# Kernel tuning notes

Hardware: AMD Instinct MI355X
Metric: run time of the kernel (lower is better)

## Reference

```python
import jax, jax.numpy as jnp
import numpy as np

PS = 32
D = 256


def setup_inputs() -> dict:
    key = jax.random.key(0)
    ks = jax.random.split(key, 9)
    B, L = 32, 32768
    s_in = 1.0 / np.sqrt(PS)
    s_d = 1.0 / np.sqrt(D)
    return {
        "x": jax.random.normal(ks[0], (B, L), dtype=jnp.float32),
        "W_proj": jax.random.normal(ks[1], (PS, D), dtype=jnp.float32) * s_in,
        "b_proj": jnp.zeros((D,), jnp.float32),
        "W_qkv": jax.random.normal(ks[2], (D, 3 * D), dtype=jnp.float32) * s_d,
        "b_qkv": jnp.zeros((3 * D,), jnp.float32),
        "W_out": jax.random.normal(ks[3], (D, D), dtype=jnp.float32) * s_d,
        "b_out": jnp.zeros((D,), jnp.float32),
        "W_head": jax.random.normal(ks[4], (D, PS), dtype=jnp.float32) * s_d,
        "b_head": jnp.zeros((PS,), jnp.float32),
    }


def reference(x, W_proj, b_proj, W_qkv, b_qkv, W_out, b_out, W_head, b_head):
    B, L = x.shape
    T = L // PS
    # InstanceNorm over full series (torch .std is unbiased -> ddof=1)
    mean = jnp.mean(x, axis=-1, keepdims=True)
    std = jnp.std(x, axis=-1, keepdims=True, ddof=1) + 1e-5
    x_norm = (x - mean) / std
    patches = x_norm.reshape(B, T, PS)
    # Patch embedding
    h = patches @ W_proj + b_proj  # [B, T, D]
    # Single-head causal self-attention (explicit scores, as in source)
    qkv = h @ W_qkv + b_qkv
    q, k, v = jnp.split(qkv, 3, axis=-1)
    scale = 1.0 / jnp.sqrt(jnp.asarray(D, dtype=h.dtype))
    attn = jnp.einsum("btd,bsd->bts", q, k) * scale  # [B, T, T]
    causal = jnp.tril(jnp.ones((T, T), dtype=bool))
    attn = jnp.where(causal, attn, -jnp.inf)
    attn = jax.nn.softmax(attn, axis=-1)
    out = jnp.einsum("bts,bsd->btd", attn, v)
    out = out @ W_out + b_out
    # Prediction head + next-patch MSE loss
    pred = out @ W_head + b_head  # [B, T, PS]
    loss = jnp.mean((pred[:, :-1] - patches[:, 1:]) ** 2)
    return loss
```

## Files before the change

### kernel.cpp

```cpp
#include <hip/hip_runtime.h>
#include <math.h>

#define B_SZ 32
#define L_SZ 32768
#define T_SZ 1024
#define PS_SZ 32
#define D_SZ 256
#define SM_M 10.0f

typedef float f32x4 __attribute__((ext_vector_type(4)));
typedef short s16x8 __attribute__((ext_vector_type(8)));
typedef unsigned short u16x8 __attribute__((ext_vector_type(8)));

__device__ __forceinline__ unsigned short f2bf(float f) {
  union { float f; unsigned int u; } v; v.f = f;
  unsigned int r = v.u + 0x7FFFu + ((v.u >> 16) & 1u);
  return (unsigned short)(r >> 16);
}

__device__ __forceinline__ void g2l16(const unsigned short* g, unsigned short* l) {
  __builtin_amdgcn_global_load_lds(
      (const __attribute__((address_space(1))) unsigned int*)g,
      (__attribute__((address_space(3))) unsigned int*)l, 16, 0, 0);
}

__global__ __launch_bounds__(256) void prep_kernel(const float* __restrict__ x,
                                                   float* __restrict__ sgpart,
                                                   const float* __restrict__ Wp,
                                                   const float* __restrict__ bp,
                                                   const float* __restrict__ Wq,
                                                   const float* __restrict__ bq,
                                                   const float* __restrict__ Wo,
                                                   const float* __restrict__ bo,
                                                   const float* __restrict__ Wh,
                                                   const float* __restrict__ bh,
                                                   float* __restrict__ Wcb,
                                                   unsigned short* __restrict__ WqT,
                                                   unsigned short* __restrict__ WfT,
                                                   float* __restrict__ bfp,
                                                   unsigned int* __restrict__ total,
                                                   float* __restrict__ lsum) {
  __shared__ float red[8];
  const int g = blockIdx.x, tid = threadIdx.x;
  const int w = tid >> 6, lane = tid & 63;
  if (g < 256) {
    const int b = g >> 3;
    const float* p = x + (size_t)b * L_SZ + (size_t)(g & 7) * 4096;
    float s = 0.f, ss = 0.f;
#pragma unroll
    for (int i = 0; i < 4; ++i) {
      float4 f = ((const float4*)p)[tid + i * 256];
      s += f.x + f.y + f.z + f.w;
      ss += f.x * f.x + f.y * f.y + f.z * f.z + f.w * f.w;
    }
#pragma unroll
    for (int off = 32; off >= 1; off >>= 1) {
      s += __shfl_down(s, off);
      ss += __shfl_down(ss, off);
    }
    if (lane == 0) { red[w] = s; red[4 + w] = ss; }
    __syncthreads();
    if (tid == 0) {
      sgpart[g * 2]     = red[0] + red[1] + red[2] + red[3];
      sgpart[g * 2 + 1] = red[4] + red[5] + red[6] + red[7];
    }
  } else if (g < 388) {
    int idx = (g - 256) * 256 + tid;
    if (idx < 33 * 768) {
      int p = idx / 768, j = idx % 768;
      const float* arow = (p < 32) ? (Wp + p * 256) : bp;
      float acc = (p < 32) ? 0.f : bq[j];
      for (int d = 0; d < 256; ++d) acc += arow[d] * Wq[d * 768 + j];
      if (p < 32) WqT[j * 32 + p] = f2bf(acc);
      else Wcb[j] = acc;
    } else {
      int k = idx - 33 * 768;
      if (k < 8192) {
        int p = k >> 8, d = k & 255;
        float acc = 0.f;
        for (int e = 0; e < 256; ++e) acc += Wo[d * 256 + e] * Wh[e * 32 + p];
        WfT[p * 256 + d] = f2bf(acc);
      } else if (k < 8224) {
        int p = k - 8192;
        float acc = bh[p];
        for (int e = 0; e < 256; ++e) acc += bo[e] * Wh[e * 32 + p];
        bfp[p] = acc;
      }
    }
  } else {
    if (tid == 0) { total[0] = 0u; lsum[0] = 0.f; }
  }
}

__global__ __launch_bounds__(256) void qkv_kernel(const float* __restrict__ x,
                                                  const float* __restrict__ sgpart,
                                                  const unsigned short* __restrict__ WqT,
                                                  const float* __restrict__ Wcb,
                                                  unsigned short* __restrict__ Qb,
                                                  unsigned short* __restrict__ Kb,
                                                  unsigned short* __restrict__ Vtt) {
  __shared__ unsigned short T4[4][8448];
  const int tid = threadIdx.x;
  const int w = tid >> 6, lane = tid & 63;
  const int lo = lane & 15, quad = lane >> 4;
  unsigned short* Tw = T4[w];
  const int mbase = blockIdx.x * 128 + w * 32;
  const int b = mbase >> 10;
  float S = 0.f, SS = 0.f;
#pragma unroll
  for (int i = 0; i < 8; ++i) {
    S += sgpart[(b * 8 + i) * 2];
    SS += sgpart[(b * 8 + i) * 2 + 1];
  }
  const float mean = S * (1.f / (float)L_SZ);
  const float var = (SS - S * mean) * (1.f / (float)(L_SZ - 1));
  const float inv = 1.f / (sqrtf(var) + 1e-5f);
  s16x8 af0, af1;
  {
    float4 a = *(const float4*)&x[(size_t)(mbase + lo) * 32 + quad * 8];
    float4 c = *(const float4*)&x[(size_t)(mbase + lo) * 32 + quad * 8 + 4];
    af0[0] = (short)f2bf((a.x - mean) * inv); af0[1] = (short)f2bf((a.y - mean) * inv);
    af0[2] = (short)f2bf((a.z - mean) * inv); af0[3] = (short)f2bf((a.w - mean) * inv);
    af0[4] = (short)f2bf((c.x - mean) * inv); af0[5] = (short)f2bf((c.y - mean) * inv);
    af0[6] = (short)f2bf((c.z - mean) * inv); af0[7] = (short)f2bf((c.w - mean) * inv);
    float4 d = *(const float4*)&x[(size_t)(mbase + 16 + lo) * 32 + quad * 8];
    float4 e = *(const float4*)&x[(size_t)(mbase + 16 + lo) * 32 + quad * 8 + 4];
    af1[0] = (short)f2bf((d.x - mean) * inv); af1[1] = (short)f2bf((d.y - mean) * inv);
    af1[2] = (short)f2bf((d.z - mean) * inv); af1[3] = (short)f2bf((d.w - mean) * inv);
    af1[4] = (short)f2bf((e.x - mean) * inv); af1[5] = (short)f2bf((e.y - mean) * inv);
    af1[6] = (short)f2bf((e.z - mean) * inv); af1[7] = (short)f2bf((e.w - mean) * inv);
  }
#pragma unroll 4
  for (int nt = 0; nt < 16; ++nt) {
    s16x8 bf = *(const s16x8*)&WqT[(size_t)(nt * 16 + lo) * 32 + quad * 8];
    f32x4 c0 = {0.f, 0.f, 0.f, 0.f}, c1 = {0.f, 0.f, 0.f, 0.f};
    c0 = __builtin_amdgcn_mfma_f32_16x16x32_bf16(af0, bf, c0, 0, 0, 0);
    c1 = __builtin_amdgcn_mfma_f32_16x16x32_bf16(af1, bf, c1, 0, 0, 0);
    const int col = nt * 16 + lo;
    const float bi = Wcb[col];
#pragma unroll
    for (int i = 0; i < 4; ++i) {
      Tw[(quad * 4 + i) * 264 + col]      = f2bf((c0[i] + bi) * 0.0625f);
      Tw[(16 + quad * 4 + i) * 264 + col] = f2bf((c1[i] + bi) * 0.0625f);
    }
  }
#pragma unroll
  for (int it = 0; it < 16; ++it) {
    const int gsub = it * 64 + lane;
    const int row = gsub >> 5, c16 = gsub & 31;
    *(u16x8*)&Qb[(size_t)(mbase + row) * 256 + c16 * 8] =
        *(const u16x8*)&Tw[row * 264 + c16 * 8];
  }
#pragma unroll 4
  for (int nt = 0; nt < 16; ++nt) {
    s16x8 bf = *(const s16x8*)&WqT[(size_t)(256 + nt * 16 + lo) * 32 + quad * 8];
    f32x4 c0 = {0.f, 0.f, 0.f, 0.f}, c1 = {0.f, 0.f, 0.f, 0.f};
    c0 = __builtin_amdgcn_mfma_f32_16x16x32_bf16(af0, bf, c0, 0, 0, 0);
    c1 = __builtin_amdgcn_mfma_f32_16x16x32_bf16(af1, bf, c1, 0, 0, 0);
    const int col = nt * 16 + lo;
    const float bi = Wcb[256 + col];
#pragma unroll
    for (int i = 0; i < 4; ++i) {
      Tw[(quad * 4 + i) * 264 + col]      = f2bf(c0[i] + bi);
      Tw[(16 + quad * 4 + i) * 264 + col] = f2bf(c1[i] + bi);
    }
  }
#pragma unroll
  for (int it = 0; it < 16; ++it) {
    const int gsub = it * 64 + lane;
    const int row = gsub >> 5, c16 = gsub & 31;
    *(u16x8*)&Kb[(size_t)(mbase + row) * 256 + c16 * 8] =
        *(const u16x8*)&Tw[row * 264 + c16 * 8];
  }
#pragma unroll 4
  for (int nt2 = 0; nt2 < 16; ++nt2) {
    s16x8 aw = *(const s16x8*)&WqT[(size_t)(512 + nt2 * 16 + lo) * 32 + quad * 8];
    f32x4 c0 = {0.f, 0.f, 0.f, 0.f}, c1 = {0.f, 0.f, 0.f, 0.f};
    c0 = __builtin_amdgcn_mfma_f32_16x16x32_bf16(aw, af0, c0, 0, 0, 0);
    c1 = __builtin_amdgcn_mfma_f32_16x16x32_bf16(aw, af1, c1, 0, 0, 0);
#pragma unroll
    for (int i = 0; i < 4; ++i) {
      const int d = nt2 * 16 + quad * 4 + i;
      const float bv = Wcb[512 + d];
      Tw[d * 32 + lo]      = f2bf(c0[i] + bv);
      Tw[d * 32 + 16 + lo] = f2bf(c1[i] + bv);
    }
  }
  {
    const int ktq = (mbase >> 5) & 31;
    const size_t vb = ((size_t)b * 32 + ktq) * 8192;
#pragma unroll
    for (int it = 0; it < 16; ++it) {
      const int gsub = it * 64 + lane;
      *(u16x8*)&Vtt[vb + gsub * 8] = *(const u16x8*)&Tw[gsub * 8];
    }
  }
}

__global__ __launch_bounds__(256) void attn_kernel(const unsigned short* __restrict__ Qb,
                                                   const unsigned short* __restrict__ Kb,
                                                   const unsigned short* __restrict__ Vtt,
                                                   const unsigned short* __restrict__ WfT,
                                                   const float* __restrict__ bfp,
                                                   const float* __restrict__ x,
                                                   const float* __restrict__ sgpart,
                                                   float* __restrict__ lsum,
                                                   unsigned int* __restrict__ total,
                                                   float* __restrict__ out) {
  __shared__ unsigned short SMEM[35328];
  const int g = blockIdx.x;
  const int j = g >> 3;
  const int b = (g & 7) * 4 + (j & 3);
  const int qt = 15 - (j >> 2);
  const int tid = threadIdx.x;
  const int w = tid >> 6, lane = tid & 63;
  const int lo = lane & 15, quad = lane >> 4;

  const int qr0 = qt * 64 + w * 16;
  const size_t kbase = (size_t)b << 10;

  s16x8 qf[8];
  const size_t qrow = (kbase + qr0 + lo) * 256;
#pragma unroll
  for (int kc = 0; kc < 8; ++kc) qf[kc] = *(const s16x8*)&Qb[qrow + kc * 32 + quad * 8];

  f32x4 O[16];
#pragma unroll
  for (int nt = 0; nt < 16; ++nt) O[nt] = (f32x4){0.f, 0.f, 0.f, 0.f};
  f32x4 Ol = {0.f, 0.f, 0.f, 0.f};
  s16x8 ones;
#pragma unroll
  for (int jj = 0; jj < 8; ++jj) ones[jj] = (short)0x3F80;

  const int c16p = tid & 31;
  const int keyr = tid >> 5;
  const int c16s = (c16p & 24) | ((c16p & 7) ^ keyr);
  const unsigned short* kgp = Kb + (kbase << 8) + keyr * 256 + c16s * 8;
  const int dql = tid >> 2;
  const int cpq = (tid & 3) ^ ((tid >> 3) & 3);
  const unsigned short* vgp = Vtt + (size_t)b * 262144 + dql * 32 + cpq * 8;
  const int ldst = (w * 64) * 8;

  unsigned short* myp = &SMEM[32768 + w * 640];
  const int lo7 = lo & 7;
  const int nk = 2 * (qt + 1);

#pragma unroll
  for (int it = 0; it < 4; ++it) g2l16(kgp + it * 2048, &SMEM[it * 2048 + ldst]);
#pragma unroll
  for (int it = 0; it < 4; ++it) g2l16(vgp + it * 2048, &SMEM[8192 + it * 2048 + ldst]);
  kgp += 8192; vgp += 8192;

  for (int kt = 0; kt < nk; ++kt) {
    const int k0 = kt * 32;
    __syncthreads();
    const int cur = (kt & 1) << 14;
    if (kt + 1 < nk) {
      const int nxt = ((kt + 1) & 1) << 14;
#pragma unroll
      for (int it = 0; it < 4; ++it) g2l16(kgp + it * 2048, &SMEM[nxt + it * 2048 + ldst]);
#pragma unroll
      for (int it = 0; it < 4; ++it)
        g2l16(vgp + it * 2048, &SMEM[nxt + 8192 + it * 2048 + ldst]);
      kgp += 8192; vgp += 8192;
    }

    if (k0 <= qr0 + 15) {
      f32x4 s0 = {0.f, 0.f, 0.f, 0.f}, s1 = {0.f, 0.f, 0.f, 0.f};
#pragma unroll
      for (int kc = 0; kc < 8; ++kc) {
        const int c16 = kc * 4 + quad;
        const int cs = (c16 & 24) | ((c16 & 7) ^ lo7);
        s16x8 kf0 = *(const s16x8*)&SMEM[cur + (lo * 32 + cs) * 8];
        s16x8 kf1 = *(const s16x8*)&SMEM[cur + ((16 + lo) * 32 + cs) * 8];
        s0 = __builtin_amdgcn_mfma_f32_16x16x32_bf16(qf[kc], kf0, s0, 0, 0, 0);
        s1 = __builtin_amdgcn_mfma_f32_16x16x32_bf16(qf[kc], kf1, s1, 0, 0, 0);
      }
      if (k0 + 31 > qr0) {
#pragma unroll
        for (int ii = 0; ii < 4; ++ii) {
          const int row = qr0 + quad * 4 + ii;
          if (k0 + lo > row) s0[ii] = -1e30f;
          if (k0 + 16 + lo > row) s1[ii] = -1e30f;
        }
      }
#pragma unroll
      for (int ii = 0; ii < 4; ++ii) {
        myp[(quad * 4 + ii) * 40 + lo]      = f2bf(__expf(s0[ii] - SM_M));
        myp[(quad * 4 + ii) * 40 + 16 + lo] = f2bf(__expf(s1[ii] - SM_M));
      }
      s16x8 pf = *(const s16x8*)&myp[lo * 40 + quad * 8];
      Ol = __builtin_amdgcn_mfma_f32_16x16x32_bf16(pf, ones, Ol, 0, 0, 0);
#pragma unroll
      for (int nt = 0; nt < 16; ++nt) {
        const int d = nt * 16 + lo;
        const int cp = quad ^ ((d >> 1) & 3);
        s16x8 vf = *(const s16x8*)&SMEM[cur + 8192 + ((d << 2) + cp) * 8];
        O[nt] = __builtin_amdgcn_mfma_f32_16x16x32_bf16(pf, vf, O[nt], 0, 0, 0);
      }
    }
  }
  __syncthreads();

  float inv4[4];
#pragma unroll
  for (int ii = 0; ii < 4; ++ii) inv4[ii] = 1.f / Ol[ii];
  unsigned short* OLw = &SMEM[w * 4224];
#pragma unroll
  for (int nt = 0; nt < 16; ++nt)
#pragma unroll
    for (int ii = 0; ii < 4; ++ii)
      OLw[(quad * 4 + ii) * 264 + nt * 16 + lo] = f2bf(O[nt][ii] * inv4[ii]);

  s16x8 af[8];
#pragma unroll
  for (int kc = 0; kc < 8; ++kc)
    af[kc] = *(const s16x8*)&OLw[lo * 264 + kc * 32 + quad * 8];

  float S = 0.f, SS = 0.f;
#pragma unroll
  for (int i = 0; i < 8; ++i) {
    S += sgpart[(b * 8 + i) * 2];
    SS += sgpart[(b * 8 + i) * 2 + 1];
  }
  const float mean = S * (1.f / (float)L_SZ);
  const float var = (SS - S * mean) * (1.f / (float)(L_SZ - 1));
  const float invb = 1.f / (sqrtf(var) + 1e-5f);

  float lacc = 0.f;
#pragma unroll
  for (int nt = 0; nt < 2; ++nt) {
    f32x4 acc = {0.f, 0.f, 0.f, 0.f};
#pragma unroll
    for (int kc = 0; kc < 8; ++kc) {
      s16x8 bfr = *(const s16x8*)&WfT[(size_t)(nt * 16 + lo) * 256 + kc * 32 + quad * 8];
      acc = __builtin_amdgcn_mfma_f32_16x16x32_bf16(af[kc], bfr, acc, 0, 0, 0);
    }
    const float ba = bfp[nt * 16 + lo];
    const int p = nt * 16 + lo;
#pragma unroll
    for (int ii = 0; ii < 4; ++ii) {
      const int t = qr0 + quad * 4 + ii;
      if (t < 1023) {
        const float pr = acc[ii] + ba;
        const float tg = (x[(size_t)b * L_SZ + (t + 1) * 32 + p] - mean) * invb;
        const float d = pr - tg;
        lacc += d * d;
      }
    }
  }
#pragma unroll
  for (int off = 32; off >= 1; off >>= 1) lacc += __shfl_down(lacc, off);
  float* redf = (float*)&SMEM[35000];
  unsigned int* flag = (unsigned int*)&SMEM[35100];
  if (lane == 0) redf[w] = lacc;
  __syncthreads();

  if (tid == 0) {
    atomicAdd(lsum, redf[0] + redf[1] + redf[2] + redf[3]);
    __threadfence();
    unsigned int prev = atomicAdd(total, 1u);
    flag[0] = (prev == 511u) ? 1u : 0u;
  }
  __syncthreads();
  if (flag[0] && tid == 0) {
    float tot = atomicAdd(lsum, 0.0f);
    out[0] = tot * (1.f / (float)(B_SZ * (T_SZ - 1) * PS_SZ));
  }
}

extern "C" void kernel_launch(void* const* d_in, const int* in_sizes, int n_in,
                              void* d_out, int out_size, void* d_ws, size_t ws_size,
                              hipStream_t stream) {
  const float* x      = (const float*)d_in[0];
  const float* W_proj = (const float*)d_in[1];
  const float* b_proj = (const float*)d_in[2];
  const float* W_qkv  = (const float*)d_in[3];
  const float* b_qkv  = (const float*)d_in[4];
  const float* W_out  = (const float*)d_in[5];
  const float* b_out  = (const float*)d_in[6];
  const float* W_head = (const float*)d_in[7];
  const float* b_head = (const float*)d_in[8];
  float* out = (float*)d_out;
  char* ws = (char*)d_ws;

  unsigned short* Qb     = (unsigned short*)ws;
  unsigned short* Kb     = (unsigned short*)(ws + (16ull << 20));
  unsigned short* Vtt    = (unsigned short*)(ws + (32ull << 20));
  char* tail = ws + (48ull << 20);
  float*          Wcb    = (float*)tail;
  unsigned short* WqT    = (unsigned short*)(tail + 4096);
  unsigned short* WfT    = (unsigned short*)(tail + 65536);
  float*          bfp    = (float*)(tail + 98304);
  float*          sgpart = (float*)(tail + 102400);
  unsigned int*   total  = (unsigned int*)(tail + 106496);
  float*          lsum   = (float*)(tail + 106496 + 64);

  prep_kernel<<<389, 256, 0, stream>>>(x, sgpart, W_proj, b_proj, W_qkv, b_qkv,
                                       W_out, b_out, W_head, b_head,
                                       Wcb, WqT, WfT, bfp, total, lsum);
  qkv_kernel<<<256, 256, 0, stream>>>(x, sgpart, WqT, Wcb, Qb, Kb, Vtt);
  attn_kernel<<<512, 256, 0, stream>>>(Qb, Kb, Vtt, WfT, bfp, x, sgpart, lsum, total, out);
}
```

Before: 161.3 us.

## Switch attention to 32x32x16 MFMA with two-wave blocks and reordered tiles

Rewrites the attention kernel so each wave handles 32 query rows using 32x32x16 bf16 MFMA instead of 16x16x32, with 128-thread blocks covering the same 64-row tile. The K, V and P tiles get new LDS swizzles, and the final head projection also uses the larger MFMA. The aim is fewer LDS fragment loads per FLOP and a better MFMA issue rate. The query-tile order across the grid is also changed, and the smaller blocks halve the waves resident per CU, which risks weaker latency hiding.

New measurement: 197.1 us. +22.2%, slower.

```diff
diff --git a/kernel.cpp b/kernel.cpp
--- a/kernel.cpp
+++ b/kernel.cpp
@@ -9,6 +9,7 @@
 #define SM_M 10.0f
 
 typedef float f32x4 __attribute__((ext_vector_type(4)));
+typedef float f32x16 __attribute__((ext_vector_type(16)));
 typedef short s16x8 __attribute__((ext_vector_type(8)));
 typedef unsigned short u16x8 __attribute__((ext_vector_type(8)));
 
@@ -197,59 +198,69 @@
   }
 }
 
-__global__ __launch_bounds__(256) void attn_kernel(const unsigned short* __restrict__ Qb,
-                                                   const unsigned short* __restrict__ Kb,
-                                                   const unsigned short* __restrict__ Vtt,
-                                                   const unsigned short* __restrict__ WfT,
-                                                   const float* __restrict__ bfp,
-                                                   const float* __restrict__ x,
-                                                   const float* __restrict__ sgpart,
-                                                   float* __restrict__ lsum,
-                                                   unsigned int* __restrict__ total,
-                                                   float* __restrict__ out) {
-  __shared__ unsigned short SMEM[35328];
+__global__ __launch_bounds__(128, 1) void attn_kernel(const unsigned short* __restrict__ Qb,
+                                                      const unsigned short* __restrict__ Kb,
+                                                      const unsigned short* __restrict__ Vtt,
+                                                      const unsigned short* __restrict__ WfT,
+                                                      const float* __restrict__ bfp,
+                                                      const float* __restrict__ x,
+                                                      const float* __restrict__ sgpart,
+                                                      float* __restrict__ lsum,
+                                                      unsigned int* __restrict__ total,
+                                                      float* __restrict__ out) {
+  __shared__ unsigned short SMEM[36352];
+  __shared__ float redf[2];
+  __shared__ unsigned int flag;
   const int g = blockIdx.x;
   const int j = g >> 3;
   const int b = (g & 7) * 4 + (j & 3);
-  const int qt = 15 - (j >> 2);
+  const int qt = (j < 32) ? (15 - (j >> 2)) : ((j - 32) >> 2);
   const int tid = threadIdx.x;
   const int w = tid >> 6, lane = tid & 63;
-  const int lo = lane & 15, quad = lane >> 4;
-
-  const int qr0 = qt * 64 + w * 16;
-  const size_t kbase = (size_t)b << 10;
-
-  s16x8 qf[8];
-  const size_t qrow = (kbase + qr0 + lo) * 256;
-#pragma unroll
-  for (int kc = 0; kc < 8; ++kc) qf[kc] = *(const s16x8*)&Qb[qrow + kc * 32 + quad * 8];
-
-  f32x4 O[16];
-#pragma unroll
-  for (int nt = 0; nt < 16; ++nt) O[nt] = (f32x4){0.f, 0.f, 0.f, 0.f};
-  f32x4 Ol = {0.f, 0.f, 0.f, 0.f};
+  const int cl = lane & 31, hi = lane >> 5;
+  const int qr0 = qt * 64 + w * 32;
+
+  s16x8 qf[16];
+  {
+    const size_t qrow = ((size_t)(b * 1024 + qr0 + cl)) * 256;
+#pragma unroll
+    for (int cb = 0; cb < 16; ++cb)
+      qf[cb] = *(const s16x8*)&Qb[qrow + cb * 16 + hi * 8];
+  }
+
+  f32x16 O[8], Ol;
+#pragma unroll
+  for (int dt = 0; dt < 8; ++dt)
+#pragma unroll
+    for (int i = 0; i < 16; ++i) O[dt][i] = 0.f;
+#pragma unroll
+  for (int i = 0; i < 16; ++i) Ol[i] = 0.f;
   s16x8 ones;
 #pragma unroll
   for (int jj = 0; jj < 8; ++jj) ones[jj] = (short)0x3F80;
 
-  const int c16p = tid & 31;
-  const int keyr = tid >> 5;
-  const int c16s = (c16p & 24) | ((c16p & 7) ^ keyr);
-  const unsigned short* kgp = Kb + (kbase << 8) + keyr * 256 + c16s * 8;
-  const int dql = tid >> 2;
-  const int cpq = (tid & 3) ^ ((tid >> 3) & 3);
-  const unsigned short* vgp = Vtt + (size_t)b * 262144 + dql * 32 + cpq * 8;
-  const int ldst = (w * 64) * 8;
-
-  unsigned short* myp = &SMEM[32768 + w * 640];
-  const int lo7 = lo & 7;
+  int kof[8];
+#pragma unroll
+  for (int it = 0; it < 8; ++it) {
+    const int key = it * 4 + (tid >> 5);
+    kof[it] = key * 256 + ((tid & 31) ^ key) * 8;
+  }
+  const int vof = (tid >> 2) * 32 + (((tid & 3) ^ ((tid >> 4) & 3))) * 8;
+  const unsigned short* KbB = Kb + (size_t)b * 262144;
+  const unsigned short* VtB = Vtt + (size_t)b * 262144;
+  const int wb = w * 512;
   const int nk = 2 * (qt + 1);
 
 #pragma unroll
-  for (int it = 0; it < 4; ++it) g2l16(kgp + it * 2048, &SMEM[it * 2048 + ldst]);
-#pragma unroll
-  for (int it = 0; it < 4; ++it) g2l16(vgp + it * 2048, &SMEM[8192 + it * 2048 + ldst]);
-  kgp += 8192; vgp += 8192;
+  for (int it = 0; it < 8; ++it) g2l16(KbB + kof[it], &SMEM[it * 1024 + wb]);
+#pragma unroll
+  for (int it = 0; it < 8; ++it) g2l16(VtB + vof + it * 1024, &SMEM[8192 + it * 1024 + wb]);
+
+  const int maskl = (cl >> 2) & 3;
+  const int cv0 = (hi ^ maskl) * 8;
+  const int cv1 = ((2 | hi) ^ maskl) * 8;
+  unsigned short* Pw = &SMEM[32768 + w * 1792];
+  const int prow = cl * 56;
 
   for (int kt = 0; kt < nk; ++kt) {
     const int k0 = kt * 32;
@@ -257,113 +268,106 @@
     const int cur = (kt & 1) << 14;
     if (kt + 1 < nk) {
       const int nxt = ((kt + 1) & 1) << 14;
-#pragma unroll
-      for (int it = 0; it < 4; ++it) g2l16(kgp + it * 2048, &SMEM[nxt + it * 2048 + ldst]);
-#pragma unroll
-      for (int it = 0; it < 4; ++it)
-        g2l16(vgp + it * 2048, &SMEM[nxt + 8192 + it * 2048 + ldst]);
-      kgp += 8192; vgp += 8192;
-    }
-
-    if (k0 <= qr0 + 15) {
-      f32x4 s0 = {0.f, 0.f, 0.f, 0.f}, s1 = {0.f, 0.f, 0.f, 0.f};
-#pragma unroll
-      for (int kc = 0; kc < 8; ++kc) {
-        const int c16 = kc * 4 + quad;
-        const int cs = (c16 & 24) | ((c16 & 7) ^ lo7);
-        s16x8 kf0 = *(const s16x8*)&SMEM[cur + (lo * 32 + cs) * 8];
-        s16x8 kf1 = *(const s16x8*)&SMEM[cur + ((16 + lo) * 32 + cs) * 8];
-        s0 = __builtin_amdgcn_mfma_f32_16x16x32_bf16(qf[kc], kf0, s0, 0, 0, 0);
-        s1 = __builtin_amdgcn_mfma_f32_16x16x32_bf16(qf[kc], kf1, s1, 0, 0, 0);
+      const int ko = (kt + 1) * 8192;
+#pragma unroll
+      for (int it = 0; it < 8; ++it) g2l16(KbB + ko + kof[it], &SMEM[nxt + it * 1024 + wb]);
+#pragma unroll
+      for (int it = 0; it < 8; ++it)
+        g2l16(VtB + ko + vof + it * 1024, &SMEM[nxt + 8192 + it * 1024 + wb]);
+    }
+
+    if (k0 <= qr0 + 31) {
+      f32x16 S;
+#pragma unroll
+      for (int i = 0; i < 16; ++i) S[i] = 0.f;
+      const int kbl = cur + cl * 256;
+#pragma unroll
+      for (int cb = 0; cb < 16; ++cb) {
+        s16x8 kf = *(const s16x8*)&SMEM[kbl + ((((cb << 1) | hi) ^ cl) << 3)];
+        S = __builtin_amdgcn_mfma_f32_32x32x16_bf16(qf[cb], kf, S, 0, 0, 0);
       }
-      if (k0 + 31 > qr0) {
-#pragma unroll
-        for (int ii = 0; ii < 4; ++ii) {
-          const int row = qr0 + quad * 4 + ii;
-          if (k0 + lo > row) s0[ii] = -1e30f;
-          if (k0 + 16 + lo > row) s1[ii] = -1e30f;
-        }
+      const bool diag = (k0 + 31 > qr0);
+#pragma unroll
+      for (int r = 0; r < 16; ++r) {
+        const int row = (r & 3) + 8 * (r >> 2) + 4 * hi;
+        float e = __expf(S[r] - SM_M);
+        if (diag && (k0 + cl > qr0 + row)) e = 0.f;
+        Pw[row * 56 + cl] = f2bf(e);
       }
-#pragma unroll
-      for (int ii = 0; ii < 4; ++ii) {
-        myp[(quad * 4 + ii) * 40 + lo]      = f2bf(__expf(s0[ii] - SM_M));
-        myp[(quad * 4 + ii) * 40 + 16 + lo] = f2bf(__expf(s1[ii] - SM_M));
+      s16x8 pf0 = *(const s16x8*)&Pw[prow + hi * 8];
+      s16x8 pf1 = *(const s16x8*)&Pw[prow + 16 + hi * 8];
+      Ol = __builtin_amdgcn_mfma_f32_32x32x16_bf16(pf0, ones, Ol, 0, 0, 0);
+      Ol = __builtin_amdgcn_mfma_f32_32x32x16_bf16(pf1, ones, Ol, 0, 0, 0);
+      const int vbl = cur + 8192 + cl * 32;
+#pragma unroll
+      for (int dt = 0; dt < 8; ++dt) {
+        s16x8 v0 = *(const s16x8*)&SMEM[vbl + dt * 1024 + cv0];
+        s16x8 v1 = *(const s16x8*)&SMEM[vbl + dt * 1024 + cv1];
+        O[dt] = __builtin_amdgcn_mfma_f32_32x32x16_bf16(pf0, v0, O[dt], 0, 0, 0);
+        O[dt] = __builtin_amdgcn_mfma_f32_32x32x16_bf16(pf1, v1, O[dt], 0, 0, 0);
       }
-      s16x8 pf = *(const s16x8*)&myp[lo * 40 + quad * 8];
-      Ol = __builtin_amdgcn_mfma_f32_16x16x32_bf16(pf, ones, Ol, 0, 0, 0);
-#pragma unroll
-      for (int nt = 0; nt < 16; ++nt) {
-        const int d = nt * 16 + lo;
-        const int cp = quad ^ ((d >> 1) & 3);
-        s16x8 vf = *(const s16x8*)&SMEM[cur + 8192 + ((d << 2) + cp) * 8];
-        O[nt] = __builtin_amdgcn_mfma_f32_16x16x32_bf16(pf, vf, O[nt], 0, 0, 0);
-      }
     }
   }
   __syncthreads();
 
-  float inv4[4];
-#pragma unroll
-  for (int ii = 0; ii < 4; ++ii) inv4[ii] = 1.f / Ol[ii];
-  unsigned short* OLw = &SMEM[w * 4224];
-#pragma unroll
-  for (int nt = 0; nt < 16; ++nt)
-#pragma unroll
-    for (int ii = 0; ii < 4; ++ii)
-      OLw[(quad * 4 + ii) * 264 + nt * 16 + lo] = f2bf(O[nt][ii] * inv4[ii]);
-
-  s16x8 af[8];
-#pragma unroll
-  for (int kc = 0; kc < 8; ++kc)
-    af[kc] = *(const s16x8*)&OLw[lo * 264 + kc * 32 + quad * 8];
-
-  float S = 0.f, SS = 0.f;
+  unsigned short* OLw = &SMEM[w * 8448];
+#pragma unroll
+  for (int r = 0; r < 16; ++r) {
+    const int row = (r & 3) + 8 * (r >> 2) + 4 * hi;
+    const float iv = 1.f / Ol[r];
+#pragma unroll
+    for (int dt = 0; dt < 8; ++dt)
+      OLw[row * 264 + dt * 32 + cl] = f2bf(O[dt][r] * iv);
+  }
+  s16x8 af[16];
+#pragma unroll
+  for (int cb = 0; cb < 16; ++cb)
+    af[cb] = *(const s16x8*)&OLw[cl * 264 + cb * 16 + hi * 8];
+
+  float S_ = 0.f, SS = 0.f;
 #pragma unroll
   for (int i = 0; i < 8; ++i) {
-    S += sgpart[(b * 8 + i) * 2];
+    S_ += sgpart[(b * 8 + i) * 2];
     SS += sgpart[(b * 8 + i) * 2 + 1];
   }
-  const float mean = S * (1.f / (float)L_SZ);
-  const float var = (SS - S * mean) * (1.f / (float)(L_SZ - 1));
+  const float mean = S_ * (1.f / (float)L_SZ);
+  const float var = (SS - S_ * mean) * (1.f / (float)(L_SZ - 1));
   const float invb = 1.f / (sqrtf(var) + 1e-5f);
 
+  f32x16 hacc;
+#pragma unroll
+  for (int i = 0; i < 16; ++i) hacc[i] = 0.f;
+#pragma unroll
+  for (int cb = 0; cb < 16; ++cb) {
+    s16x8 bfr = *(const s16x8*)&WfT[(size_t)cl * 256 + cb * 16 + hi * 8];
+    hacc = __builtin_amdgcn_mfma_f32_32x32x16_bf16(af[cb], bfr, hacc, 0, 0, 0);
+  }
+  const float ba = bfp[cl];
   float lacc = 0.f;
 #pragma unroll
-  for (int nt = 0; nt < 2; ++nt) {
-    f32x4 acc = {0.f, 0.f, 0.f, 0.f};
-#pragma unroll
-    for (int kc = 0; kc < 8; ++kc) {
-      s16x8 bfr = *(const s16x8*)&WfT[(size_t)(nt * 16 + lo) * 256 + kc * 32 + quad * 8];
-      acc = __builtin_amdgcn_mfma_f32_16x16x32_bf16(af[kc], bfr, acc, 0, 0, 0);
-    }
-    const float ba = bfp[nt * 16 + lo];
-    const int p = nt * 16 + lo;
-#pragma unroll
-    for (int ii = 0; ii < 4; ++ii) {
-      const int t = qr0 + quad * 4 + ii;
-      if (t < 1023) {
-        const float pr = acc[ii] + ba;
-        const float tg = (x[(size_t)b * L_SZ + (t + 1) * 32 + p] - mean) * invb;
-        const float d = pr - tg;
-        lacc += d * d;
-      }
+  for (int r = 0; r < 16; ++r) {
+    const int row = (r & 3) + 8 * (r >> 2) + 4 * hi;
+    const int t = qr0 + row;
+    if (t < 1023) {
+      const float pr = hacc[r] + ba;
+      const float tg = (x[(size_t)b * L_SZ + (t + 1) * 32 + cl] - mean) * invb;
+      const float d = pr - tg;
+      lacc += d * d;
     }
   }
 #pragma unroll
   for (int off = 32; off >= 1; off >>= 1) lacc += __shfl_down(lacc, off);
-  float* redf = (float*)&SMEM[35000];
-  unsigned int* flag = (unsigned int*)&SMEM[35100];
   if (lane == 0) redf[w] = lacc;
   __syncthreads();
 
   if (tid == 0) {
-    atomicAdd(lsum, redf[0] + redf[1] + redf[2] + redf[3]);
+    atomicAdd(lsum, redf[0] + redf[1]);
     __threadfence();
     unsigned int prev = atomicAdd(total, 1u);
-    flag[0] = (prev == 511u) ? 1u : 0u;
+    flag = (prev == 511u) ? 1u : 0u;
   }
   __syncthreads();
-  if (flag[0] && tid == 0) {
+  if (flag && tid == 0) {
     float tot = atomicAdd(lsum, 0.0f);
     out[0] = tot * (1.f / (float)(B_SZ * (T_SZ - 1) * PS_SZ));
   }
@@ -400,5 +404,5 @@
                                        W_out, b_out, W_head, b_head,
                                        Wcb, WqT, WfT, bfp, total, lsum);
   qkv_kernel<<<256, 256, 0, stream>>>(x, sgpart, WqT, Wcb, Qb, Kb, Vtt);
-  attn_kernel<<<512, 256, 0, stream>>>(Qb, Kb, Vtt, WfT, bfp, x, sgpart, lsum, total, out);
-}
+  attn_kernel<<<512, 128, 0, stream>>>(Qb, Kb, Vtt, WfT, bfp, x, sgpart, lsum, total, out);
+}
```
